# Kernel optimization log

Hardware: AMD Instinct MI355X
Metric: run time of the kernel (lower is better)

The kernel has to match this reference:

```python
import jax, jax.numpy as jnp
import numpy as np

D = 512
H = 8
DK = D // H
FF = 4 * D
EPS = 1e-5
NEG = -1.0e9


def _layernorm(x, g, b):
    mu = jnp.mean(x, axis=-1, keepdims=True)
    var = jnp.mean((x - mu) ** 2, axis=-1, keepdims=True)
    return (x - mu) * jax.lax.rsqrt(var + EPS) * g + b


def setup_inputs() -> dict:
    key = jax.random.key(0)
    ks = jax.random.split(key, 16)
    B, S = 4, 2048
    x = jax.random.normal(ks[0], (B, S, D), dtype=jnp.float32)
    # causal mask, broadcastable to [B, H, S, S]; mask==0 -> blocked
    mask = jnp.tril(jnp.ones((S, S), dtype=jnp.int32))[None, None]
    s = 1.0 / np.sqrt(D)
    sf = 1.0 / np.sqrt(FF)
    p = {
        "wq": jax.random.normal(ks[1], (D, D), jnp.float32) * s,
        "bq": jnp.zeros((D,), jnp.float32),
        "wk": jax.random.normal(ks[2], (D, D), jnp.float32) * s,
        "bk": jnp.zeros((D,), jnp.float32),
        "wv": jax.random.normal(ks[3], (D, D), jnp.float32) * s,
        "bv": jnp.zeros((D,), jnp.float32),
        "wo": jax.random.normal(ks[4], (D, D), jnp.float32) * s,
        "bo": jnp.zeros((D,), jnp.float32),
        "w1": jax.random.normal(ks[5], (D, FF), jnp.float32) * s,
        "b1": jnp.zeros((FF,), jnp.float32),
        "w2": jax.random.normal(ks[6], (FF, D), jnp.float32) * sf,
        "b2": jnp.zeros((D,), jnp.float32),
        "g1": jnp.ones((D,), jnp.float32),
        "be1": jnp.zeros((D,), jnp.float32),
        "g2": jnp.ones((D,), jnp.float32),
        "be2": jnp.zeros((D,), jnp.float32),
    }
    return {"x": x, "mask": mask, **p}


def reference(x, mask, wq, bq, wk, bk, wv, bv, wo, bo, w1, b1, w2, b2, g1, be1, g2, be2):
    B, S, _ = x.shape
    # projections -> [B, H, S, DK]
    q = (x @ wq + bq).reshape(B, S, H, DK).transpose(0, 2, 1, 3)
    k = (x @ wk + bk).reshape(B, S, H, DK).transpose(0, 2, 1, 3)
    v = (x @ wv + bv).reshape(B, S, H, DK).transpose(0, 2, 1, 3)
    scores = jnp.einsum("bhqd,bhkd->bhqk", q, k) / np.sqrt(DK)
    scores = jnp.where(mask == 0, NEG, scores)
    attn = jax.nn.softmax(scores, axis=-1)
    ctx = jnp.einsum("bhqk,bhkd->bhqd", attn, v)
    ctx = ctx.transpose(0, 2, 1, 3).reshape(B, S, D)
    attn_out = ctx @ wo + bo
    # dropout is inference-mode identity
    h = _layernorm(x + attn_out, g1, be1)
    ffn = jax.nn.relu(h @ w1 + b1) @ w2 + b2
    return _layernorm(h + ffn, g2, be2)
```

## Files before the change

### kernel.cpp

```cpp
#include <hip/hip_runtime.h>
#include <math.h>

#define D_   512
#define H_   8
#define DK_  64
#define FF_  2048
#define S_   2048
#define B_   4
#define M_   (B_*S_)
#define EPS_ 1e-5f
#define SCLQ 0.1803368801111f

typedef __attribute__((ext_vector_type(8))) short bf16x8;
typedef __attribute__((ext_vector_type(4))) short bf16x4;
typedef __attribute__((ext_vector_type(4))) float f32x4;
typedef __attribute__((ext_vector_type(4))) unsigned int u32x4;

__device__ inline unsigned short f2b(float f) {
    unsigned u = __builtin_bit_cast(unsigned, f);
    unsigned r = (u + 0x7FFFu + ((u >> 16) & 1u)) >> 16;
    return (unsigned short)r;
}
__device__ inline float b2f(unsigned short u) {
    return __builtin_bit_cast(float, (unsigned)u << 16);
}
__device__ inline unsigned packbf(float p0, float p1) {
    unsigned r;
    asm("v_cvt_pk_bf16_f32 %0, %1, %2" : "=v"(r) : "v"(p0), "v"(p1));
    return r;
}

__device__ __forceinline__ void async_cp16(const void* g, void* l) {
    __builtin_amdgcn_global_load_lds(
        (const __attribute__((address_space(1))) unsigned int*)g,
        (__attribute__((address_space(3))) unsigned int*)l, 16, 0, 0);
}

__global__ __launch_bounds__(256)
void prep_kernel(const float* __restrict__ x,
                 const float* __restrict__ wq, const float* __restrict__ wk,
                 const float* __restrict__ wv, const float* __restrict__ wo,
                 const float* __restrict__ bq, const float* __restrict__ bk,
                 const float* __restrict__ bv,
                 const float* __restrict__ w1, const float* __restrict__ w2,
                 unsigned short* __restrict__ xb, unsigned short* __restrict__ wqkvt,
                 unsigned short* __restrict__ wot, unsigned short* __restrict__ w1t,
                 unsigned short* __restrict__ w2t, float* __restrict__ bqkv)
{
    __shared__ float L[32][33];
    const int bid = blockIdx.x;
    const int tid = threadIdx.x;

    if (bid < 2048) {
        const int i = (bid * 256 + tid) * 8;
        const float4 a = *(const float4*)(x + i);
        const float4 b = *(const float4*)(x + i + 4);
        bf16x8 v;
        v[0] = (short)f2b(a.x); v[1] = (short)f2b(a.y);
        v[2] = (short)f2b(a.z); v[3] = (short)f2b(a.w);
        v[4] = (short)f2b(b.x); v[5] = (short)f2b(b.y);
        v[6] = (short)f2b(b.z); v[7] = (short)f2b(b.w);
        *(bf16x8*)(xb + i) = v;
        return;
    }

    const float* w; unsigned short* wt; int K, N, k0, n0; float scl = 1.f;
    if (bid < 3072) {
        const int z = (bid - 2048) >> 8;
        const int r = (bid - 2048) & 255;
        n0 = (r & 15) * 32; k0 = (r >> 4) * 32; K = 512; N = 512;
        w  = (z == 0) ? wq : (z == 1) ? wk : (z == 2) ? wv : wo;
        wt = (z < 3) ? (wqkvt + (size_t)z * 512 * 512) : wot;
        if (z == 0) scl = SCLQ;
        if (z < 3 && r == 0) {
            const float* bsrc = (z == 0) ? bq : (z == 1) ? bk : bv;
            const float bscl  = (z == 0) ? SCLQ : 1.f;
            bqkv[z * 512 + tid]       = bsrc[tid] * bscl;
            bqkv[z * 512 + 256 + tid] = bsrc[256 + tid] * bscl;
        }
    } else if (bid < 4096) {
        const int r = bid - 3072;
        n0 = (r & 63) * 32; k0 = (r >> 6) * 32; K = 512; N = 2048;
        w = w1; wt = w1t;
    } else {
        const int r = bid - 4096;
        n0 = (r & 15) * 32; k0 = (r >> 4) * 32; K = 2048; N = 512;
        w = w2; wt = w2t;
    }

    const int xx = tid & 31, y = tid >> 5;
#pragma unroll
    for (int i = 0; i < 4; i++)
        L[y + i * 8][xx] = w[(size_t)(k0 + y + i * 8) * N + n0 + xx] * scl;
    __syncthreads();
#pragma unroll
    for (int i = 0; i < 4; i++)
        wt[(size_t)(n0 + y + i * 8) * K + k0 + xx] = f2b(L[xx][y + i * 8]);
}

template<int WR, int WC, int MT, int NT, int BK, int OUTB, int RELU, int RESADD, int HASBIAS>
__global__ __launch_bounds__(256)
void gemm_bf16(const unsigned short* __restrict__ A, const unsigned short* __restrict__ Bt,
               const float* __restrict__ bias, const void* __restrict__ RES,
               void* __restrict__ Cv, int K, int lda, int ldb, int ldc)
{
    constexpr int BM  = WR * MT * 16;
    constexpr int BN  = WC * NT * 16;
    constexpr int CPR = BK / 8;
    constexpr int CA  = BM * BK / (256 * 8);
    constexpr int CB  = BN * BK / (256 * 8);
    __shared__ unsigned short As[2][BM * BK];
    __shared__ unsigned short Bs[2][BN * BK];

    const int tid  = threadIdx.x;
    const int lane = tid & 63;
    const int w    = tid >> 6;
    const int wr   = w / WC, wc = w % WC;
    const int quad = lane >> 4;
    const int l15  = lane & 15;
    const int n0   = blockIdx.x * BN;
    const int m0   = blockIdx.y * BM;

    f32x4 acc[MT][NT];
#pragma unroll
    for (int i = 0; i < MT; i++)
#pragma unroll
        for (int j = 0; j < NT; j++) acc[i][j] = (f32x4){0.f, 0.f, 0.f, 0.f};

    auto stage = [&](int k0, int bufi) {
#pragma unroll
        for (int i = 0; i < CA; i++) {
            const int c   = tid + i * 256;
            const int row = c / CPR;
            int l = c % CPR;
            if (BK == 64) l ^= (row & 7);
            async_cp16(&A[(size_t)(m0 + row) * lda + k0 + l * 8], &As[bufi][c * 8]);
        }
#pragma unroll
        for (int i = 0; i < CB; i++) {
            const int c   = tid + i * 256;
            const int row = c / CPR;
            int l = c % CPR;
            if (BK == 64) l ^= (row & 7);
            async_cp16(&Bt[(size_t)(n0 + row) * ldb + k0 + l * 8], &Bs[bufi][c * 8]);
        }
    };

    stage(0, 0);
    const int niter = K / BK;
    for (int ii = 0; ii < niter; ii++) {
        const int knext = (ii + 1 < niter) ? (ii + 1) * BK : 0;
        stage(knext, (ii + 1) & 1);
        __builtin_amdgcn_s_waitcnt(0x0f70 | (CA + CB));
        __builtin_amdgcn_s_barrier();

        const unsigned short* Ac = &As[ii & 1][0];
        const unsigned short* Bc = &Bs[ii & 1][0];
#pragma unroll
        for (int ks = 0; ks < BK / 32; ks++) {
            bf16x8 af[MT], bfr[NT];
#pragma unroll
            for (int t = 0; t < MT; t++) {
                const int r = wr * MT * 16 + t * 16 + l15;
                int ch = (ks << 2) | quad;
                if (BK == 64) ch ^= (r & 7);
                af[t] = *(const bf16x8*)&Ac[r * BK + ch * 8];
            }
#pragma unroll
            for (int t = 0; t < NT; t++) {
                const int r = wc * NT * 16 + t * 16 + l15;
                int ch = (ks << 2) | quad;
                if (BK == 64) ch ^= (r & 7);
                bfr[t] = *(const bf16x8*)&Bc[r * BK + ch * 8];
            }
#pragma unroll
            for (int mt = 0; mt < MT; mt++)
#pragma unroll
                for (int nt = 0; nt < NT; nt++)
                    acc[mt][nt] = __builtin_amdgcn_mfma_f32_16x16x32_bf16(
                        af[mt], bfr[nt], acc[mt][nt], 0, 0, 0);
        }
        __builtin_amdgcn_s_barrier();
    }

#pragma unroll
    for (int mt = 0; mt < MT; mt++) {
        const int rowb = m0 + wr * MT * 16 + mt * 16 + quad * 4;
#pragma unroll
        for (int nt = 0; nt < NT; nt++) {
            const int col = n0 + wc * NT * 16 + nt * 16 + l15;
            const float bv = HASBIAS ? bias[col] : 0.f;
#pragma unroll
            for (int r = 0; r < 4; r++) {
                const size_t idx = (size_t)(rowb + r) * ldc + col;
                float v = acc[mt][nt][r] + bv;
                if (RESADD == 1) v += ((const float*)RES)[idx];
                if (RESADD == 2) v += b2f(((const unsigned short*)RES)[idx]);
                if (RELU)   v = fmaxf(v, 0.f);
                if (OUTB) ((unsigned short*)Cv)[idx] = f2b(v);
                else      ((float*)Cv)[idx] = v;
            }
        }
    }
}

__global__ __launch_bounds__(256)
void vtrans(const unsigned short* __restrict__ qkv, unsigned short* __restrict__ vt)
{
    __shared__ unsigned short L[64][72];
    const int s0 = blockIdx.x * 64;
    const int bh = blockIdx.y;
    const int b  = bh >> 3, hh = bh & 7;
    const int tid = threadIdx.x;
    const unsigned short* src = qkv + (size_t)(b * S_) * 1536 + 1024 + hh * 64;
#pragma unroll
    for (int i = 0; i < 2; i++) {
        const int c = tid + i * 256;
        const int r = c >> 3, sub = (c & 7) * 8;
        *(bf16x8*)&L[r][sub] = *(const bf16x8*)(src + (size_t)(s0 + r) * 1536 + sub);
    }
    __syncthreads();
    const int dk = tid >> 2;
    const int sc = (tid & 3) * 16;
    bf16x8 t0, t1;
#pragma unroll
    for (int j = 0; j < 8; j++) t0[j] = (short)L[sc + j][dk];
#pragma unroll
    for (int j = 0; j < 8; j++) t1[j] = (short)L[sc + 8 + j][dk];
    unsigned short* dst = vt + (size_t)(bh * 64 + dk) * S_ + s0 + sc;
    *(bf16x8*)(dst)     = t0;
    *(bf16x8*)(dst + 8) = t1;
}

__global__ __launch_bounds__(256, 4)
void attn_mfma(const unsigned short* __restrict__ qkv,
               const unsigned short* __restrict__ vt,
               unsigned short* __restrict__ ctx)
{
    __shared__ unsigned short Arena[16384];

    const int tid  = threadIdx.x;
    const int lane = tid & 63;
    const int w    = tid >> 6;
    const int quad = lane >> 4;
    const int l15  = lane & 15;
    const int bid  = blockIdx.x;
    const int g    = bid >> 5;
    const int qb   = (g < 8) ? 31 - g : (g < 16) ? g + 8 : (g < 24) ? 31 - g : g - 24;
    const int bh   = bid & 31;
    const int b    = bh >> 3, hh = bh & 7;
    const int kh   = w & 1;
    const int qh   = w >> 1;

    const unsigned short* qbase = qkv + (size_t)(b * S_) * 1536 + hh * 64;
    const unsigned short* kbase = qbase + 512;
    const unsigned short* vtb   = vt + (size_t)bh * 64 * S_;

    bf16x4 ones4;
#pragma unroll
    for (int j = 0; j < 4; j++) ones4[j] = (short)0x3F80;

    auto stage = [&](int kb, int bufi) {
        unsigned short* kd = &Arena[bufi * 4096];
        unsigned short* vd = &Arena[8192 + bufi * 4096];
#pragma unroll
        for (int i = 0; i < 2; i++) {
            const int c = tid + i * 256;
            const int row = c >> 3;
            const int l = (c & 7) ^ (row & 7);
            async_cp16(kbase + (size_t)(kb * 64 + row) * 1536 + l * 8, kd + c * 8);
            async_cp16(vtb + (size_t)row * S_ + kb * 64 + l * 8, vd + c * 8);
        }
    };

    bf16x8 qf[2][2];
#pragma unroll
    for (int qt = 0; qt < 2; qt++) {
        const unsigned short* qr = qbase + (size_t)(qb * 64 + qh * 32 + qt * 16 + l15) * 1536;
        qf[qt][0] = *(const bf16x8*)(qr + quad * 8);
        qf[qt][1] = *(const bf16x8*)(qr + 32 + quad * 8);
    }

    f32x4 Oacc[2][5];
#pragma unroll
    for (int qt = 0; qt < 2; qt++)
#pragma unroll
        for (int i = 0; i < 5; i++) Oacc[qt][i] = (f32x4){0.f, 0.f, 0.f, 0.f};

    stage(0, 0);

    const int vch0 = (kh * 4 + (quad >> 1));
    const int vsub = (quad & 1) * 4;

    for (int kb = 0; kb < qb; kb++) {
        stage(kb + 1, (kb + 1) & 1);
        __builtin_amdgcn_s_waitcnt(0x0F74);
        __builtin_amdgcn_s_barrier();
        const unsigned short* Kc = &Arena[(kb & 1) * 4096];
        const unsigned short* Vc = &Arena[8192 + (kb & 1) * 4096];

        f32x4 st[2][2];
#pragma unroll
        for (int qt = 0; qt < 2; qt++)
#pragma unroll
            for (int kt = 0; kt < 2; kt++) st[qt][kt] = (f32x4){0.f, 0.f, 0.f, 0.f};
#pragma unroll
        for (int kc = 0; kc < 2; kc++) {
            const int phys = (kc * 4 + quad) ^ (l15 & 7);
            const bf16x8 kf0 = *(const bf16x8*)&Kc[(kh * 32 + l15) * 64 + phys * 8];
            const bf16x8 kf1 = *(const bf16x8*)&Kc[(kh * 32 + 16 + l15) * 64 + phys * 8];
#pragma unroll
            for (int qt = 0; qt < 2; qt++) {
                st[qt][0] = __builtin_amdgcn_mfma_f32_16x16x32_bf16(kf0, qf[qt][kc], st[qt][0], 0, 0, 0);
                st[qt][1] = __builtin_amdgcn_mfma_f32_16x16x32_bf16(kf1, qf[qt][kc], st[qt][1], 0, 0, 0);
            }
        }

        bf16x4 vf[2][4];
#pragma unroll
        for (int kt = 0; kt < 2; kt++)
#pragma unroll
            for (int nt = 0; nt < 4; nt++)
                vf[kt][nt] = *(const bf16x4*)&Vc[(nt * 16 + l15) * 64 +
                    (((vch0 + kt * 2) ^ (l15 & 7)) << 3) + vsub];

#pragma unroll
        for (int qt = 0; qt < 2; qt++) {
#pragma unroll
            for (int kt = 0; kt < 2; kt++) {
                uint2 aw;
                aw.x = packbf(exp2f(st[qt][kt][0]), exp2f(st[qt][kt][1]));
                aw.y = packbf(exp2f(st[qt][kt][2]), exp2f(st[qt][kt][3]));
                const bf16x4 af = __builtin_bit_cast(bf16x4, aw);
#pragma unroll
                for (int nt = 0; nt < 4; nt++)
                    Oacc[qt][nt] = __builtin_amdgcn_mfma_f32_16x16x16bf16_1k(
                        af, vf[kt][nt], Oacc[qt][nt], 0, 0, 0);
                Oacc[qt][4] = __builtin_amdgcn_mfma_f32_16x16x16bf16_1k(
                    af, ones4, Oacc[qt][4], 0, 0, 0);
            }
        }
        __builtin_amdgcn_s_barrier();
    }

    {
        stage(0, (qb + 1) & 1);
        __builtin_amdgcn_s_waitcnt(0x0F74);
        __builtin_amdgcn_s_barrier();
        const unsigned short* Kc = &Arena[(qb & 1) * 4096];
        const unsigned short* Vc = &Arena[8192 + (qb & 1) * 4096];

        const bool skipDiag = (kh == 1 && qh == 0);
        const bool fullDiag = (kh == 0 && qh == 1);

        if (!skipDiag) {
            f32x4 st[2][2];
#pragma unroll
            for (int qt = 0; qt < 2; qt++)
#pragma unroll
                for (int kt = 0; kt < 2; kt++) st[qt][kt] = (f32x4){0.f, 0.f, 0.f, 0.f};
#pragma unroll
            for (int kc = 0; kc < 2; kc++) {
                const int phys = (kc * 4 + quad) ^ (l15 & 7);
                const bf16x8 kf0 = *(const bf16x8*)&Kc[(kh * 32 + l15) * 64 + phys * 8];
                const bf16x8 kf1 = *(const bf16x8*)&Kc[(kh * 32 + 16 + l15) * 64 + phys * 8];
#pragma unroll
                for (int qt = 0; qt < 2; qt++) {
                    st[qt][0] = __builtin_amdgcn_mfma_f32_16x16x32_bf16(kf0, qf[qt][kc], st[qt][0], 0, 0, 0);
                    st[qt][1] = __builtin_amdgcn_mfma_f32_16x16x32_bf16(kf1, qf[qt][kc], st[qt][1], 0, 0, 0);
                }
            }

            bf16x4 af[2][2];
            if (fullDiag) {
#pragma unroll
                for (int qt = 0; qt < 2; qt++)
#pragma unroll
                    for (int kt = 0; kt < 2; kt++) {
                        uint2 aw;
                        aw.x = packbf(exp2f(st[qt][kt][0]), exp2f(st[qt][kt][1]));
                        aw.y = packbf(exp2f(st[qt][kt][2]), exp2f(st[qt][kt][3]));
                        af[qt][kt] = __builtin_bit_cast(bf16x4, aw);
                    }
            } else {
                float p[4];
                uint2 aw;
#pragma unroll
                for (int r = 0; r < 4; r++)
                    p[r] = (quad * 4 + r > l15) ? 0.f : exp2f(st[0][0][r]);
                aw.x = packbf(p[0], p[1]); aw.y = packbf(p[2], p[3]);
                af[0][0] = __builtin_bit_cast(bf16x4, aw);
                af[0][1] = (bf16x4){0, 0, 0, 0};
                aw.x = packbf(exp2f(st[1][0][0]), exp2f(st[1][0][1]));
                aw.y = packbf(exp2f(st[1][0][2]), exp2f(st[1][0][3]));
                af[1][0] = __builtin_bit_cast(bf16x4, aw);
#pragma unroll
                for (int r = 0; r < 4; r++)
                    p[r] = (quad * 4 + r > l15) ? 0.f : exp2f(st[1][1][r]);
                aw.x = packbf(p[0], p[1]); aw.y = packbf(p[2], p[3]);
                af[1][1] = __builtin_bit_cast(bf16x4, aw);
            }

            bf16x4 vf[2][4];
#pragma unroll
            for (int kt = 0; kt < 2; kt++)
#pragma unroll
                for (int nt = 0; nt < 4; nt++)
                    vf[kt][nt] = *(const bf16x4*)&Vc[(nt * 16 + l15) * 64 +
                        (((vch0 + kt * 2) ^ (l15 & 7)) << 3) + vsub];

#pragma unroll
            for (int qt = 0; qt < 2; qt++)
#pragma unroll
                for (int kt = 0; kt < 2; kt++) {
#pragma unroll
                    for (int nt = 0; nt < 4; nt++)
                        Oacc[qt][nt] = __builtin_amdgcn_mfma_f32_16x16x16bf16_1k(
                            af[qt][kt], vf[kt][nt], Oacc[qt][nt], 0, 0, 0);
                    Oacc[qt][4] = __builtin_amdgcn_mfma_f32_16x16x16bf16_1k(
                        af[qt][kt], ones4, Oacc[qt][4], 0, 0, 0);
                }
        }
    }

    __syncthreads();
    float* red = (float*)&Arena[0];
    const int rbase = (qh * 64 + lane) * 44;
    if (kh) {
#pragma unroll
        for (int qt = 0; qt < 2; qt++)
#pragma unroll
            for (int i = 0; i < 5; i++)
                *(f32x4*)&red[rbase + (qt * 5 + i) * 4] = Oacc[qt][i];
    }
    __syncthreads();
    if (!kh) {
#pragma unroll
        for (int qt = 0; qt < 2; qt++)
#pragma unroll
            for (int i = 0; i < 5; i++)
                Oacc[qt][i] += *(const f32x4*)&red[rbase + (qt * 5 + i) * 4];

        unsigned short* cb = ctx + (size_t)(b * S_) * 512 + hh * 64;
#pragma unroll
        for (int qt = 0; qt < 2; qt++) {
            const int orow = qb * 64 + qh * 32 + qt * 16 + quad * 4;
#pragma unroll
            for (int r = 0; r < 4; r++) {
                const float inv = 1.f / Oacc[qt][4][r];
#pragma unroll
                for (int nt = 0; nt < 4; nt++)
                    cb[(size_t)(orow + r) * 512 + nt * 16 + l15] = f2b(Oacc[qt][nt][r] * inv);
            }
        }
    }
}

template<int WF, int WB>
__global__ __launch_bounds__(256)
void ln_kernel(const float* __restrict__ s, const float* __restrict__ g,
               const float* __restrict__ be, float* __restrict__ out,
               unsigned short* __restrict__ outb)
{
    const int wave = threadIdx.x >> 6;
    const int lane = threadIdx.x & 63;
    const int row  = blockIdx.x * 4 + wave;
    const float* ps = s + (size_t)row * D_;
    const int c0 = lane * 4;

    float v[8];
    {
        const float4 a0 = *(const float4*)(ps + c0);
        const float4 a1 = *(const float4*)(ps + c0 + 256);
        v[0] = a0.x; v[1] = a0.y; v[2] = a0.z; v[3] = a0.w;
        v[4] = a1.x; v[5] = a1.y; v[6] = a1.z; v[7] = a1.w;
    }

    float sum = 0.f;
#pragma unroll
    for (int i = 0; i < 8; i++) sum += v[i];
#pragma unroll
    for (int m = 1; m < 64; m <<= 1) sum += __shfl_xor(sum, m);
    const float mu = sum * (1.f / D_);

    float sq = 0.f;
#pragma unroll
    for (int i = 0; i < 8; i++) { const float d = v[i] - mu; sq += d * d; }
#pragma unroll
    for (int m = 1; m < 64; m <<= 1) sq += __shfl_xor(sq, m);
    const float rstd = rsqrtf(sq * (1.f / D_) + EPS_);

    const float4 g0 = *(const float4*)(g + c0);
    const float4 b0 = *(const float4*)(be + c0);
    const float4 g1 = *(const float4*)(g + c0 + 256);
    const float4 b1 = *(const float4*)(be + c0 + 256);

    float o[8];
    o[0] = (v[0] - mu) * rstd * g0.x + b0.x;
    o[1] = (v[1] - mu) * rstd * g0.y + b0.y;
    o[2] = (v[2] - mu) * rstd * g0.z + b0.z;
    o[3] = (v[3] - mu) * rstd * g0.w + b0.w;
    o[4] = (v[4] - mu) * rstd * g1.x + b1.x;
    o[5] = (v[5] - mu) * rstd * g1.y + b1.y;
    o[6] = (v[6] - mu) * rstd * g1.z + b1.z;
    o[7] = (v[7] - mu) * rstd * g1.w + b1.w;

    if (WF) {
        *(float4*)(out + (size_t)row * D_ + c0)       = *(float4*)&o[0];
        *(float4*)(out + (size_t)row * D_ + c0 + 256) = *(float4*)&o[4];
    }
    if (WB) {
        short4 vb0 = (short4){(short)f2b(o[0]), (short)f2b(o[1]), (short)f2b(o[2]), (short)f2b(o[3])};
        short4 vb1 = (short4){(short)f2b(o[4]), (short)f2b(o[5]), (short)f2b(o[6]), (short)f2b(o[7])};
        *(short4*)(outb + (size_t)row * D_ + c0)       = vb0;
        *(short4*)(outb + (size_t)row * D_ + c0 + 256) = vb1;
    }
}

extern "C" void kernel_launch(void* const* d_in, const int* in_sizes, int n_in,
                              void* d_out, int out_size, void* d_ws, size_t ws_size,
                              hipStream_t stream)
{
    const float* x  = (const float*)d_in[0];
    const float* wq = (const float*)d_in[2];
    const float* bq = (const float*)d_in[3];
    const float* wk = (const float*)d_in[4];
    const float* bk = (const float*)d_in[5];
    const float* wv = (const float*)d_in[6];
    const float* bv = (const float*)d_in[7];
    const float* wo = (const float*)d_in[8];
    const float* bo = (const float*)d_in[9];
    const float* w1 = (const float*)d_in[10];
    const float* b1 = (const float*)d_in[11];
    const float* w2 = (const float*)d_in[12];
    const float* b2 = (const float*)d_in[13];
    const float* g1 = (const float*)d_in[14];
    const float* be1= (const float*)d_in[15];
    const float* g2 = (const float*)d_in[16];
    const float* be2= (const float*)d_in[17];
    float* out = (float*)d_out;

    const size_t MB = 1048576;
    char* w8 = (char*)d_ws;
    unsigned short* wqkvt = (unsigned short*)(w8 + 0);
    unsigned short* wot   = (unsigned short*)(w8 + 1572864);
    unsigned short* w1t   = (unsigned short*)(w8 + 2097152);
    unsigned short* w2t   = (unsigned short*)(w8 + 4194304);
    float*          bqkv  = (float*)(w8 + 6291456);
    unsigned short* qkv   = (unsigned short*)(w8 + 8 * MB);
    unsigned short* ffn1b = qkv;
    unsigned short* xb    = (unsigned short*)(w8 + 40 * MB);
    unsigned short* ctx   = xb;
    unsigned short* vt    = (unsigned short*)(w8 + 48 * MB);
    unsigned short* hb    = vt;
    float*          pre   = (float*)(w8 + 56 * MB);

    const dim3 blk(256);

    prep_kernel<<<dim3(5120), blk, 0, stream>>>(
        x, wq, wk, wv, wo, bq, bk, bv, w1, w2, xb, wqkvt, wot, w1t, w2t, bqkv);

    gemm_bf16<2,2,2,4,64,1,0,0,1><<<dim3(12, 128), blk, 0, stream>>>(
        xb, wqkvt, bqkv, nullptr, qkv, 512, 512, 512, 1536);

    vtrans<<<dim3(32, 32), blk, 0, stream>>>(qkv, vt);

    attn_mfma<<<dim3(1024), blk, 0, stream>>>(qkv, vt, ctx);

    gemm_bf16<2,2,2,4,64,0,0,1,1><<<dim3(4, 128), blk, 0, stream>>>(
        ctx, wot, bo, x, pre, 512, 512, 512, 512);

    ln_kernel<1,1><<<dim3(M_ / 4), blk, 0, stream>>>(pre, g1, be1, pre, hb);

    gemm_bf16<2,2,2,4,64,1,1,0,1><<<dim3(16, 128), blk, 0, stream>>>(
        hb, w1t, b1, nullptr, ffn1b, 512, 512, 512, 2048);

    gemm_bf16<2,2,2,4,64,0,0,1,1><<<dim3(4, 128), blk, 0, stream>>>(
        ffn1b, w2t, b2, pre, pre, 2048, 2048, 2048, 512);

    ln_kernel<1,0><<<dim3(M_ / 4), blk, 0, stream>>>(pre, g2, be2, out, nullptr);
}
```

Measured before the change: 264.3 us.

## Fuse V transpose into QKV GEMM epilogue and use bf16 residual for FFN

```diff
diff --git a/kernel.cpp b/kernel.cpp
--- a/kernel.cpp
+++ b/kernel.cpp
@@ -98,11 +98,12 @@
         wt[(size_t)(n0 + y + i * 8) * K + k0 + xx] = f2b(L[xx][y + i * 8]);
 }
 
-template<int WR, int WC, int MT, int NT, int BK, int OUTB, int RELU, int RESADD, int HASBIAS>
+template<int WR, int WC, int MT, int NT, int BK, int OUTB, int RELU, int RESADD, int HASBIAS, int VT>
 __global__ __launch_bounds__(256)
 void gemm_bf16(const unsigned short* __restrict__ A, const unsigned short* __restrict__ Bt,
                const float* __restrict__ bias, const void* __restrict__ RES,
-               void* __restrict__ Cv, int K, int lda, int ldb, int ldc)
+               void* __restrict__ Cv, unsigned short* __restrict__ vtout,
+               int K, int lda, int ldb, int ldc)
 {
     constexpr int BM  = WR * MT * 16;
     constexpr int BN  = WC * NT * 16;
@@ -190,46 +191,28 @@
         for (int nt = 0; nt < NT; nt++) {
             const int col = n0 + wc * NT * 16 + nt * 16 + l15;
             const float bv = HASBIAS ? bias[col] : 0.f;
-#pragma unroll
-            for (int r = 0; r < 4; r++) {
-                const size_t idx = (size_t)(rowb + r) * ldc + col;
-                float v = acc[mt][nt][r] + bv;
-                if (RESADD == 1) v += ((const float*)RES)[idx];
-                if (RESADD == 2) v += b2f(((const unsigned short*)RES)[idx]);
-                if (RELU)   v = fmaxf(v, 0.f);
-                if (OUTB) ((unsigned short*)Cv)[idx] = f2b(v);
-                else      ((float*)Cv)[idx] = v;
-            }
-        }
-    }
-}
-
-__global__ __launch_bounds__(256)
-void vtrans(const unsigned short* __restrict__ qkv, unsigned short* __restrict__ vt)
-{
-    __shared__ unsigned short L[64][72];
-    const int s0 = blockIdx.x * 64;
-    const int bh = blockIdx.y;
-    const int b  = bh >> 3, hh = bh & 7;
-    const int tid = threadIdx.x;
-    const unsigned short* src = qkv + (size_t)(b * S_) * 1536 + 1024 + hh * 64;
-#pragma unroll
-    for (int i = 0; i < 2; i++) {
-        const int c = tid + i * 256;
-        const int r = c >> 3, sub = (c & 7) * 8;
-        *(bf16x8*)&L[r][sub] = *(const bf16x8*)(src + (size_t)(s0 + r) * 1536 + sub);
-    }
-    __syncthreads();
-    const int dk = tid >> 2;
-    const int sc = (tid & 3) * 16;
-    bf16x8 t0, t1;
-#pragma unroll
-    for (int j = 0; j < 8; j++) t0[j] = (short)L[sc + j][dk];
-#pragma unroll
-    for (int j = 0; j < 8; j++) t1[j] = (short)L[sc + 8 + j][dk];
-    unsigned short* dst = vt + (size_t)(bh * 64 + dk) * S_ + s0 + sc;
-    *(bf16x8*)(dst)     = t0;
-    *(bf16x8*)(dst + 8) = t1;
+            if (VT && col >= 1024) {
+                short4 sv;
+                sv.x = (short)f2b(acc[mt][nt][0] + bv);
+                sv.y = (short)f2b(acc[mt][nt][1] + bv);
+                sv.z = (short)f2b(acc[mt][nt][2] + bv);
+                sv.w = (short)f2b(acc[mt][nt][3] + bv);
+                const int bb = rowb >> 11;
+                *(short4*)&vtout[(size_t)(bb * 512 + (col - 1024)) * S_ + (rowb & 2047)] = sv;
+            } else {
+#pragma unroll
+                for (int r = 0; r < 4; r++) {
+                    const size_t idx = (size_t)(rowb + r) * ldc + col;
+                    float v = acc[mt][nt][r] + bv;
+                    if (RESADD == 1) v += ((const float*)RES)[idx];
+                    if (RESADD == 2) v += b2f(((const unsigned short*)RES)[idx]);
+                    if (RELU)   v = fmaxf(v, 0.f);
+                    if (OUTB) ((unsigned short*)Cv)[idx] = f2b(v);
+                    else      ((float*)Cv)[idx] = v;
+                }
+            }
+        }
+    }
 }
 
 __global__ __launch_bounds__(256, 4)
@@ -560,23 +543,21 @@
     prep_kernel<<<dim3(5120), blk, 0, stream>>>(
         x, wq, wk, wv, wo, bq, bk, bv, w1, w2, xb, wqkvt, wot, w1t, w2t, bqkv);
 
-    gemm_bf16<2,2,2,4,64,1,0,0,1><<<dim3(12, 128), blk, 0, stream>>>(
-        xb, wqkvt, bqkv, nullptr, qkv, 512, 512, 512, 1536);
-
-    vtrans<<<dim3(32, 32), blk, 0, stream>>>(qkv, vt);
+    gemm_bf16<2,2,2,4,64,1,0,0,1,1><<<dim3(12, 128), blk, 0, stream>>>(
+        xb, wqkvt, bqkv, nullptr, qkv, vt, 512, 512, 512, 1536);
 
     attn_mfma<<<dim3(1024), blk, 0, stream>>>(qkv, vt, ctx);
 
-    gemm_bf16<2,2,2,4,64,0,0,1,1><<<dim3(4, 128), blk, 0, stream>>>(
-        ctx, wot, bo, x, pre, 512, 512, 512, 512);
-
-    ln_kernel<1,1><<<dim3(M_ / 4), blk, 0, stream>>>(pre, g1, be1, pre, hb);
-
-    gemm_bf16<2,2,2,4,64,1,1,0,1><<<dim3(16, 128), blk, 0, stream>>>(
-        hb, w1t, b1, nullptr, ffn1b, 512, 512, 512, 2048);
-
-    gemm_bf16<2,2,2,4,64,0,0,1,1><<<dim3(4, 128), blk, 0, stream>>>(
-        ffn1b, w2t, b2, pre, pre, 2048, 2048, 2048, 512);
+    gemm_bf16<2,2,2,4,64,0,0,1,1,0><<<dim3(4, 128), blk, 0, stream>>>(
+        ctx, wot, bo, x, pre, nullptr, 512, 512, 512, 512);
+
+    ln_kernel<0,1><<<dim3(M_ / 4), blk, 0, stream>>>(pre, g1, be1, nullptr, hb);
+
+    gemm_bf16<2,2,2,4,64,1,1,0,1,0><<<dim3(16, 128), blk, 0, stream>>>(
+        hb, w1t, b1, nullptr, ffn1b, nullptr, 512, 512, 512, 2048);
+
+    gemm_bf16<2,2,2,4,64,0,0,2,1,0><<<dim3(4, 128), blk, 0, stream>>>(
+        ffn1b, w2t, b2, hb, pre, nullptr, 2048, 2048, 2048, 512);
 
     ln_kernel<1,0><<<dim3(M_ / 4), blk, 0, stream>>>(pre, g2, be2, out, nullptr);
 }
```

Result: faster. 257.0 us, median of 2 (-2.7%).
